# Kernel optimization log

Measured on AMD Instinct MI355X. Metric: run time of the kernel, lower is better.

## Reference

```python
import jax, jax.numpy as jnp
import numpy as np

NEG_BIG = -9.0e15  # matches torch's -9000000000000000.0 mask fill
ALPHA = 0.2        # leakyrelu negative slope


def setup_inputs() -> dict:
    key = jax.random.key(0)
    k1, k2, k3, k4, k5 = jax.random.split(key, 5)
    N, F_in, F_out = 4096, 512, 64
    stdv = 1.0 / np.sqrt(F_out)
    x = jax.random.normal(k1, (N, F_in), dtype=jnp.float32)
    adj = jax.random.randint(k2, (N, N), 0, 2, dtype=jnp.int32)
    W = jax.random.uniform(k3, (F_in, F_out), dtype=jnp.float32, minval=-stdv, maxval=stdv)
    a = jax.random.normal(k4, (2 * F_out, 1), dtype=jnp.float32) * 0.1
    bias = jax.random.uniform(k5, (F_out,), dtype=jnp.float32, minval=-stdv, maxval=stdv)
    return {"x": x, "adj": adj, "W": W, "a": a, "bias": bias}


def _gat_forward(x, adj, W, a, bias):
    N = x.shape[0]
    F_out = W.shape[1]
    h = x @ W  # (N, F)
    a1 = a[:F_out, 0]   # weights hitting the first concat half
    a2 = a[F_out:, 0]   # weights hitting the second concat half
    # First half: row k=i*N+j of the concat holds h_j  ->  e1[j] = h_j . a1
    e1 = h @ a1  # (N,)
    # Second half of this repo's concat is NOT h_i; exact index algebra:
    # second[k=i*N+j, r] = h[(r*N+i)//F, (((r*N+i)%F)*N + j) % F]
    # Since it depends on j only via j % F, build table T[i, t] (t = j % F).
    r = jnp.arange(F_out)[:, None]          # (F, 1)
    i = jnp.arange(N)[None, :]              # (1, N)
    m = r * N + i                           # (F, N)
    p = m // F_out                          # row index into h
    s0 = m % F_out
    t = jnp.arange(F_out)                   # (F,)
    col = (s0[..., None] * N + t) % F_out   # (F, N, F) column index into h
    vals = h[p[..., None], col]             # (F, N, F)
    T = jnp.einsum('r,rit->it', a2, vals)   # (N, F)
    j = jnp.arange(N)
    e2 = T[:, j % F_out]                    # (N, N) second-half contribution
    e = e1[None, :] + e2                    # (N, N) pre-activation scores
    e = jnp.where(e > 0, e, ALPHA * e)      # LeakyReLU(0.2)
    e = jnp.where(adj > 0, e, NEG_BIG)      # mask non-edges
    att = jax.nn.softmax(e, axis=1)         # row-wise softmax (dropout = eval identity)
    out = jax.nn.relu(att @ h) + bias       # relu BEFORE bias add, as in source
    return out


def reference(x, adj, W, a, bias):
    return _gat_forward(x, adj, W, a, bias)
```

## Files before the change

### kernel.cpp

```cpp
#include <hip/hip_runtime.h>
#include <math.h>

#define N_NODES 4096
#define F_IN    512
#define F_OUT   64
#define ALPHA   0.2f
#define NPART   8

typedef _Float16 half8 __attribute__((ext_vector_type(8)));
typedef _Float16 half4 __attribute__((ext_vector_type(4)));
typedef float    floatx4 __attribute__((ext_vector_type(4)));

union H8U4 { half8 h; uint32_t u[4]; };

__device__ __forceinline__ void async_copy16(void* lds, const void* g) {
    __builtin_amdgcn_global_load_lds(
        (const __attribute__((address_space(1))) unsigned int*)g,
        (__attribute__((address_space(3))) unsigned int*)lds, 16, 0, 0);
}

__global__ __launch_bounds__(256) void k_prep2(const float* __restrict__ W,
                                               _Float16* __restrict__ WT,
                                               const int* __restrict__ adj,
                                               uint32_t* __restrict__ bm) {
    int gb = blockIdx.x;
    if (gb < 2048) {
        int wid = gb * 256 + threadIdx.x;
        const int* p = adj + (size_t)wid * 32;
        uint32_t m = 0;
#pragma unroll
        for (int q = 0; q < 8; ++q) {
            int4 v = *(const int4*)(p + q * 4);
            m |= (v.x > 0 ? 1u : 0u) << (q * 4 + 0);
            m |= (v.y > 0 ? 1u : 0u) << (q * 4 + 1);
            m |= (v.z > 0 ? 1u : 0u) << (q * 4 + 2);
            m |= (v.w > 0 ? 1u : 0u) << (q * 4 + 3);
        }
        bm[wid] = m;
    } else {
        int idx = (gb - 2048) * 256 + threadIdx.x;
        int t = idx >> 9;
        int k = idx & 511;
        WT[idx] = (_Float16)W[k * F_OUT + t];
    }
}

__global__ __launch_bounds__(512) void k_hW(const float* __restrict__ x,
                                            const _Float16* __restrict__ WT,
                                            const float* __restrict__ a,
                                            float* __restrict__ h,
                                            _Float16* __restrict__ hT,
                                            float* __restrict__ e1) {
    __shared__ float red[8][16][64];
    int tid  = threadIdx.x;
    int lane = tid & 63;
    int w    = tid >> 6;
    int i0   = blockIdx.x * 16;
    int n    = lane & 15;
    int quad = lane >> 4;

    floatx4 acc[4] = {{0,0,0,0},{0,0,0,0},{0,0,0,0},{0,0,0,0}};

    const float* xr = x + (size_t)(i0 + n) * F_IN + w * 64 + quad * 8;
    const _Float16* wb = WT + w * 64 + quad * 8;
#pragma unroll
    for (int kk = 0; kk < 64; kk += 32) {
        float4 x0 = *(const float4*)(xr + kk);
        float4 x1 = *(const float4*)(xr + kk + 4);
        half8 af = {(_Float16)x0.x, (_Float16)x0.y, (_Float16)x0.z, (_Float16)x0.w,
                    (_Float16)x1.x, (_Float16)x1.y, (_Float16)x1.z, (_Float16)x1.w};
#pragma unroll
        for (int g = 0; g < 4; ++g) {
            half8 bf = *(const half8*)(wb + (size_t)(g * 16 + n) * F_IN + kk);
            acc[g] = __builtin_amdgcn_mfma_f32_16x16x32_f16(af, bf, acc[g], 0, 0, 0);
        }
    }
#pragma unroll
    for (int g = 0; g < 4; ++g)
#pragma unroll
        for (int r = 0; r < 4; ++r)
            red[w][g * 4 + r][lane] = acc[g][r];
    __syncthreads();
    if (w != 0) return;
#pragma unroll
    for (int g = 0; g < 4; ++g)
#pragma unroll
        for (int r = 0; r < 4; ++r) {
            float v = 0.f;
#pragma unroll
            for (int ww = 0; ww < 8; ++ww)
                v += red[ww][g * 4 + r][lane];
            acc[g][r] = v;
        }
#pragma unroll
    for (int g = 0; g < 4; ++g) {
        half4 hv;
#pragma unroll
        for (int r = 0; r < 4; ++r) {
            h[(size_t)(i0 + quad * 4 + r) * F_OUT + g * 16 + n] = acc[g][r];
            hv[r] = (_Float16)acc[g][r];
        }
        *(half4*)(hT + (size_t)(g * 16 + n) * N_NODES + i0 + quad * 4) = hv;
    }
    float a1v[4];
#pragma unroll
    for (int g = 0; g < 4; ++g) a1v[g] = a[g * 16 + n];
#pragma unroll
    for (int r = 0; r < 4; ++r) {
        float v = acc[0][r] * a1v[0] + acc[1][r] * a1v[1] + acc[2][r] * a1v[2] + acc[3][r] * a1v[3];
        v += __shfl_xor(v, 1, 64);
        v += __shfl_xor(v, 2, 64);
        v += __shfl_xor(v, 4, 64);
        v += __shfl_xor(v, 8, 64);
        if (n == 0) e1[i0 + quad * 4 + r] = v;
    }
}

__global__ __launch_bounds__(256, 3) void k_main(const uint32_t* __restrict__ bm,
                                                 const float* __restrict__ h,
                                                 const float* __restrict__ e1,
                                                 const float* __restrict__ a,
                                                 const _Float16* __restrict__ hT,
                                                 float* __restrict__ out_part,
                                                 float* __restrict__ den_part) {
    __shared__ _Float16 lds_B[16][512];
    __shared__ _Float16 lds_P[512];
    __shared__ float    lds_part[4][64];
    __shared__ float    TqS[64];

    int tid  = threadIdx.x;
    int lane = tid & 63;
    int w    = tid >> 6;
    int b    = blockIdx.x;
    int rb   = b >> 3;
    int s    = b & 7;
    int i0   = rb * 64 + w * 16;
    int n    = lane & 15;
    int quad = lane >> 4;

    const uint32_t* bmr = bm + (size_t)(i0 + n) * (N_NODES / 32) + s * 16;
    uint4 bwa = *(const uint4*)(bmr + 0);
    uint4 bwb = *(const uint4*)(bmr + 4);
    uint4 bwc = *(const uint4*)(bmr + 8);
    uint4 bwd = *(const uint4*)(bmr + 12);
    uint32_t bw[16] = {bwa.x, bwa.y, bwa.z, bwa.w, bwb.x, bwb.y, bwb.z, bwb.w,
                       bwc.x, bwc.y, bwc.z, bwc.w, bwd.x, bwd.y, bwd.z, bwd.w};

    {
        int t  = tid & 63;
        int rp = tid >> 6;
        const float* a2 = a + F_OUT;
        float ssum = 0.f;
#pragma unroll
        for (int rr = 0; rr < 16; ++rr) {
            int r = rp * 16 + rr;
            ssum += a2[r] * h[(size_t)r * 4096 + rb * 64 + t];
        }
        lds_part[rp][t] = ssum;
    }
    __syncthreads();
    if (tid < 64)
        TqS[tid] = lds_part[0][tid] + lds_part[1][tid] + lds_part[2][tid] + lds_part[3][tid];
    __syncthreads();
    {
        int j = s * 512 + tid * 2;
        float2 ev = *(const float2*)(e1 + j);
        float e0 = ev.x + TqS[(tid * 2) & 63];
        float e1v = ev.y + TqS[(tid * 2 + 1) & 63];
        e0  = e0  > 0.f ? e0  : ALPHA * e0;
        e1v = e1v > 0.f ? e1v : ALPHA * e1v;
        lds_P[tid * 2]     = (_Float16)__expf(e0);
        lds_P[tid * 2 + 1] = (_Float16)__expf(e1v);
    }

    floatx4 acc[4] = {{0,0,0,0},{0,0,0,0},{0,0,0,0},{0,0,0,0}};
    floatx4 accd = {0, 0, 0, 0};
    _Float16 one_h = (n == 0) ? (_Float16)1.0f : (_Float16)0.0f;
    half8 ones_f = {one_h, one_h, one_h, one_h, one_h, one_h, one_h, one_h};

#pragma unroll
    for (int it = 0; it < 4; ++it) {
        int jb = s * 512 + it * 128;
        const _Float16* hT_base = hT + (size_t)(w * 16 + n) * N_NODES + jb + quad * 8;
#pragma unroll
        for (int c = 0; c < 4; ++c)
            async_copy16(&lds_B[w * 4 + c][0], hT_base + c * 32);
        __syncthreads();

#pragma unroll
        for (int c = 0; c < 4; ++c) {
            uint32_t mbyte = bw[it * 4 + c] >> (quad * 8);
            H8U4 pv, af;
            pv.h = *(const half8*)&lds_P[it * 128 + c * 32 + quad * 8];
            af.u[0] = pv.u[0] & (((mbyte &   1u) ? 0x0000FFFFu : 0u) | ((mbyte &   2u) ? 0xFFFF0000u : 0u));
            af.u[1] = pv.u[1] & (((mbyte &   4u) ? 0x0000FFFFu : 0u) | ((mbyte &   8u) ? 0xFFFF0000u : 0u));
            af.u[2] = pv.u[2] & (((mbyte &  16u) ? 0x0000FFFFu : 0u) | ((mbyte &  32u) ? 0xFFFF0000u : 0u));
            af.u[3] = pv.u[3] & (((mbyte &  64u) ? 0x0000FFFFu : 0u) | ((mbyte & 128u) ? 0xFFFF0000u : 0u));
#pragma unroll
            for (int g4 = 0; g4 < 4; ++g4) {
                half8 bf = *(const half8*)&lds_B[g4 * 4 + c][lane * 8];
                acc[g4] = __builtin_amdgcn_mfma_f32_16x16x32_f16(af.h, bf, acc[g4], 0, 0, 0);
            }
            accd = __builtin_amdgcn_mfma_f32_16x16x32_f16(af.h, ones_f, accd, 0, 0, 0);
        }
        __syncthreads();
    }

    float* op = out_part + ((size_t)s * N_NODES + i0) * F_OUT;
#pragma unroll
    for (int g4 = 0; g4 < 4; ++g4)
#pragma unroll
        for (int r = 0; r < 4; ++r)
            op[(quad * 4 + r) * F_OUT + g4 * 16 + n] = acc[g4][r];
    if (n == 0) {
#pragma unroll
        for (int r = 0; r < 4; ++r)
            den_part[s * N_NODES + i0 + quad * 4 + r] = accd[r];
    }
}

__global__ __launch_bounds__(128) void k_out(const float* __restrict__ out_part,
                                             const float* __restrict__ den_part,
                                             const float* __restrict__ bias,
                                             float* __restrict__ out) {
    int idx4 = blockIdx.x * 128 + threadIdx.x;
    int base = idx4 * 4;
    int i = base >> 6;
    int t = base & 63;
    float4 sacc = {0.f, 0.f, 0.f, 0.f};
    float dacc = 0.f;
#pragma unroll
    for (int p = 0; p < NPART; ++p) {
        float4 v = ((const float4*)(out_part + (size_t)p * N_NODES * F_OUT))[idx4];
        sacc.x += v.x; sacc.y += v.y; sacc.z += v.z; sacc.w += v.w;
        dacc += den_part[p * N_NODES + i];
    }
    float4 bv = *(const float4*)(bias + t);
    float4 o;
    o.x = fmaxf(sacc.x / dacc, 0.f) + bv.x;
    o.y = fmaxf(sacc.y / dacc, 0.f) + bv.y;
    o.z = fmaxf(sacc.z / dacc, 0.f) + bv.z;
    o.w = fmaxf(sacc.w / dacc, 0.f) + bv.w;
    ((float4*)out)[idx4] = o;
}

extern "C" void kernel_launch(void* const* d_in, const int* in_sizes, int n_in,
                              void* d_out, int out_size, void* d_ws, size_t ws_size,
                              hipStream_t stream) {
    const float* x    = (const float*)d_in[0];
    const int*   adj  = (const int*)d_in[1];
    const float* W    = (const float*)d_in[2];
    const float* a    = (const float*)d_in[3];
    const float* bias = (const float*)d_in[4];
    float* out = (float*)d_out;

    char* ws = (char*)d_ws;
    float*    h        = (float*)ws;
    _Float16* hT       = (_Float16*)(ws + 1024 * 1024);
    float*    e1       = (float*)(ws + 1536 * 1024);
    _Float16* WT       = (_Float16*)(ws + 1552 * 1024);
    uint32_t* bm       = (uint32_t*)(ws + 2128 * 1024);
    float*    out_part = (float*)(ws + 4176 * 1024);
    float*    den_part = (float*)(ws + (4176 + 8192) * 1024);

    k_prep2<<<2176, 256, 0, stream>>>(W, WT, adj, bm);
    k_hW   <<<256, 512, 0, stream>>>(x, WT, a, h, hT, e1);
    k_main <<<512, 256, 0, stream>>>(bm, h, e1, a, hT, out_part, den_part);
    k_out  <<<512, 128, 0, stream>>>(out_part, den_part, bias, out);
}
```

Before: 122.0 us.

## Fuse adjacency bitmask and h=xW into one kernel, prefetch all hT tiles upfront

```diff
diff --git a/kernel.cpp b/kernel.cpp
--- a/kernel.cpp
+++ b/kernel.cpp
@@ -19,13 +19,20 @@
         (__attribute__((address_space(3))) unsigned int*)lds, 16, 0, 0);
 }
 
-__global__ __launch_bounds__(256) void k_prep2(const float* __restrict__ W,
-                                               _Float16* __restrict__ WT,
-                                               const int* __restrict__ adj,
-                                               uint32_t* __restrict__ bm) {
-    int gb = blockIdx.x;
-    if (gb < 2048) {
-        int wid = gb * 256 + threadIdx.x;
+__global__ __launch_bounds__(512) void k_pre(const float* __restrict__ x,
+                                             const int* __restrict__ adj,
+                                             const float* __restrict__ W,
+                                             const float* __restrict__ a,
+                                             uint32_t* __restrict__ bm,
+                                             float* __restrict__ h,
+                                             _Float16* __restrict__ hT,
+                                             float* __restrict__ e1) {
+    __shared__ float red[8][16][64];
+    int gb  = blockIdx.x;
+    int tid = threadIdx.x;
+
+    if (gb < 1024) {
+        int wid = gb * 512 + tid;
         const int* p = adj + (size_t)wid * 32;
         uint32_t m = 0;
 #pragma unroll
@@ -37,41 +44,30 @@
             m |= (v.w > 0 ? 1u : 0u) << (q * 4 + 3);
         }
         bm[wid] = m;
-    } else {
-        int idx = (gb - 2048) * 256 + threadIdx.x;
-        int t = idx >> 9;
-        int k = idx & 511;
-        WT[idx] = (_Float16)W[k * F_OUT + t];
-    }
-}
-
-__global__ __launch_bounds__(512) void k_hW(const float* __restrict__ x,
-                                            const _Float16* __restrict__ WT,
-                                            const float* __restrict__ a,
-                                            float* __restrict__ h,
-                                            _Float16* __restrict__ hT,
-                                            float* __restrict__ e1) {
-    __shared__ float red[8][16][64];
-    int tid  = threadIdx.x;
+        return;
+    }
+
     int lane = tid & 63;
     int w    = tid >> 6;
-    int i0   = blockIdx.x * 16;
+    int i0   = (gb - 1024) * 16;
     int n    = lane & 15;
     int quad = lane >> 4;
 
     floatx4 acc[4] = {{0,0,0,0},{0,0,0,0},{0,0,0,0},{0,0,0,0}};
 
     const float* xr = x + (size_t)(i0 + n) * F_IN + w * 64 + quad * 8;
-    const _Float16* wb = WT + w * 64 + quad * 8;
 #pragma unroll
     for (int kk = 0; kk < 64; kk += 32) {
         float4 x0 = *(const float4*)(xr + kk);
         float4 x1 = *(const float4*)(xr + kk + 4);
         half8 af = {(_Float16)x0.x, (_Float16)x0.y, (_Float16)x0.z, (_Float16)x0.w,
                     (_Float16)x1.x, (_Float16)x1.y, (_Float16)x1.z, (_Float16)x1.w};
+        int k0 = w * 64 + kk + quad * 8;
 #pragma unroll
         for (int g = 0; g < 4; ++g) {
-            half8 bf = *(const half8*)(wb + (size_t)(g * 16 + n) * F_IN + kk);
+            const float* wc = W + (size_t)k0 * F_OUT + g * 16 + n;
+            half8 bf = {(_Float16)wc[0 * 64], (_Float16)wc[1 * 64], (_Float16)wc[2 * 64], (_Float16)wc[3 * 64],
+                        (_Float16)wc[4 * 64], (_Float16)wc[5 * 64], (_Float16)wc[6 * 64], (_Float16)wc[7 * 64]};
             acc[g] = __builtin_amdgcn_mfma_f32_16x16x32_f16(af, bf, acc[g], 0, 0, 0);
         }
     }
@@ -116,14 +112,14 @@
     }
 }
 
-__global__ __launch_bounds__(256, 3) void k_main(const uint32_t* __restrict__ bm,
+__global__ __launch_bounds__(256, 2) void k_main(const uint32_t* __restrict__ bm,
                                                  const float* __restrict__ h,
                                                  const float* __restrict__ e1,
                                                  const float* __restrict__ a,
                                                  const _Float16* __restrict__ hT,
                                                  float* __restrict__ out_part,
                                                  float* __restrict__ den_part) {
-    __shared__ _Float16 lds_B[16][512];
+    __shared__ _Float16 lds_B[4][16][512];
     __shared__ _Float16 lds_P[512];
     __shared__ float    lds_part[4][64];
     __shared__ float    TqS[64];
@@ -138,6 +134,15 @@
     int n    = lane & 15;
     int quad = lane >> 4;
 
+#pragma unroll
+    for (int it = 0; it < 4; ++it) {
+        int jb = s * 512 + it * 128;
+        const _Float16* hT_base = hT + (size_t)(w * 16 + n) * N_NODES + jb + quad * 8;
+#pragma unroll
+        for (int c = 0; c < 4; ++c)
+            async_copy16(&lds_B[it][w * 4 + c][0], hT_base + c * 32);
+    }
+
     const uint32_t* bmr = bm + (size_t)(i0 + n) * (N_NODES / 32) + s * 16;
     uint4 bwa = *(const uint4*)(bmr + 0);
     uint4 bwb = *(const uint4*)(bmr + 4);
@@ -172,6 +177,7 @@
         lds_P[tid * 2]     = (_Float16)__expf(e0);
         lds_P[tid * 2 + 1] = (_Float16)__expf(e1v);
     }
+    __syncthreads();
 
     floatx4 acc[4] = {{0,0,0,0},{0,0,0,0},{0,0,0,0},{0,0,0,0}};
     floatx4 accd = {0, 0, 0, 0};
@@ -180,13 +186,6 @@
 
 #pragma unroll
     for (int it = 0; it < 4; ++it) {
-        int jb = s * 512 + it * 128;
-        const _Float16* hT_base = hT + (size_t)(w * 16 + n) * N_NODES + jb + quad * 8;
-#pragma unroll
-        for (int c = 0; c < 4; ++c)
-            async_copy16(&lds_B[w * 4 + c][0], hT_base + c * 32);
-        __syncthreads();
-
 #pragma unroll
         for (int c = 0; c < 4; ++c) {
             uint32_t mbyte = bw[it * 4 + c] >> (quad * 8);
@@ -198,12 +197,11 @@
             af.u[3] = pv.u[3] & (((mbyte &  64u) ? 0x0000FFFFu : 0u) | ((mbyte & 128u) ? 0xFFFF0000u : 0u));
 #pragma unroll
             for (int g4 = 0; g4 < 4; ++g4) {
-                half8 bf = *(const half8*)&lds_B[g4 * 4 + c][lane * 8];
+                half8 bf = *(const half8*)&lds_B[it][g4 * 4 + c][lane * 8];
                 acc[g4] = __builtin_amdgcn_mfma_f32_16x16x32_f16(af.h, bf, acc[g4], 0, 0, 0);
             }
             accd = __builtin_amdgcn_mfma_f32_16x16x32_f16(af.h, ones_f, accd, 0, 0, 0);
         }
-        __syncthreads();
     }
 
     float* op = out_part + ((size_t)s * N_NODES + i0) * F_OUT;
@@ -258,13 +256,11 @@
     float*    h        = (float*)ws;
     _Float16* hT       = (_Float16*)(ws + 1024 * 1024);
     float*    e1       = (float*)(ws + 1536 * 1024);
-    _Float16* WT       = (_Float16*)(ws + 1552 * 1024);
     uint32_t* bm       = (uint32_t*)(ws + 2128 * 1024);
     float*    out_part = (float*)(ws + 4176 * 1024);
     float*    den_part = (float*)(ws + (4176 + 8192) * 1024);
 
-    k_prep2<<<2176, 256, 0, stream>>>(W, WT, adj, bm);
-    k_hW   <<<256, 512, 0, stream>>>(x, WT, a, h, hT, e1);
-    k_main <<<512, 256, 0, stream>>>(bm, h, e1, a, hT, out_part, den_part);
-    k_out  <<<512, 128, 0, stream>>>(out_part, den_part, bias, out);
-}
+    k_pre <<<1280, 512, 0, stream>>>(x, adj, W, a, bm, h, hT, e1);
+    k_main<<<512, 256, 0, stream>>>(bm, h, e1, a, hT, out_part, den_part);
+    k_out <<<512, 128, 0, stream>>>(out_part, den_part, bias, out);
+}
```

New measurement: 120.9 us. No clear change (-0.8%).
